# Kernel tuning notes

Measured on AMD Instinct MI355X. Metric: run time of the kernel, lower is better.

## Reference

```python
import jax, jax.numpy as jnp
import numpy as np

MU = 5
ITERATIONS = 3


def _sobel(x):
    # torch kernel: stack([K, K.T]) with K = vertical-gradient Sobel; conv2d is cross-correlation
    k = jnp.array([[-1., -2., -1.], [0., 0., 0.], [1., 2., 1.]], dtype=x.dtype)
    kern = jnp.stack([k, k.T])[:, None]  # [2,1,3,3] -> channels (Gy, Gx)
    return jax.lax.conv_general_dilated(
        x, kern, window_strides=(1, 1), padding=[(1, 1), (1, 1)],
        dimension_numbers=("NCHW", "OIHW", "NCHW"))


def _normalize(v):
    # norm over channel dim, zeros replaced by 1 (matches tang_mag[tang_mag==0]=1)
    mag = jnp.linalg.norm(v, axis=1, keepdims=True)
    mag = jnp.where(mag == 0, jnp.ones_like(mag), mag)
    return v / mag


def etf_forward(inputs, mu=MU, iterations=ITERATIONS):
    B, _, H, W = inputs.shape
    sobel = _sobel(inputs)                                   # [B,2,H,W]
    sobel_mag = jnp.linalg.norm(sobel, axis=1, keepdims=True)
    sobel_mag = sobel_mag / jnp.max(sobel_mag)               # [B,1,H,W]
    pad = lambda t: jnp.pad(t, ((0, 0), (0, 0), (mu, mu), (mu, mu)))
    sobel_mag_padded = pad(sobel_mag)
    sobel_X = sobel_mag
    # tang = sobel.flip(channels) * [-1, 1] => [-Gx, Gy], then normalized
    tang = jnp.stack([-sobel[:, 1], sobel[:, 0]], axis=1)
    tang = _normalize(tang)
    for _ in range(iterations):
        for ori in ("Vertical", "Horizontal"):
            tang_padded = pad(tang)
            tang_X = tang
            acc = jnp.zeros_like(tang)
            for i in range(2 * mu + 1):
                if ori == "Vertical":
                    tang_Y = tang_padded[:, :, i:i + H, mu:mu + W]
                    sobel_Y = sobel_mag_padded[:, :, i:i + H, mu:mu + W]
                else:
                    tang_Y = tang_padded[:, :, mu:mu + H, i:i + W]
                    sobel_Y = sobel_mag_padded[:, :, mu:mu + H, i:i + W]
                w = (jnp.tanh(sobel_Y - sobel_X) + 1.0) * jnp.sum(tang_X * tang_Y, axis=1, keepdims=True) * 0.5
                acc = acc + tang_Y * w
            tang = _normalize(acc)
    return tang


def setup_inputs() -> dict:
    key = jax.random.key(0)
    inputs = jax.random.uniform(key, (2, 1, 1024, 1024), dtype=jnp.float32)
    return {"inputs": inputs}


def reference(inputs) -> jnp.ndarray:
    return etf_forward(inputs)
```

## Files before the change

### kernel.cpp

```cpp
#include <hip/hip_runtime.h>

#define BB 2
#define HH 1024
#define WW 1024
#define MU 5

#define TH 32
#define TW 64
#define SH (TH + 2 * MU)
#define SCW 80
#define SMS 83
#define SVS 81

__device__ __forceinline__ float fast_rcp(float x) { return __builtin_amdgcn_rcpf(x); }
__device__ __forceinline__ float fast_rsq(float x) { return __builtin_amdgcn_rsqf(x); }

#define SR 8
__global__ __launch_bounds__(256) void sobel_init(
    const float* __restrict__ x,
    float* __restrict__ tf,
    float* __restrict__ mag,
    float* __restrict__ block_max)
{
    __shared__ float xs[SR + 2][264];
    const int t = threadIdx.x;
    const int w0 = blockIdx.x * 256;
    const int h0 = blockIdx.y * SR;
    const int b = blockIdx.z;
    const size_t plane = (size_t)HH * WW;
    const float* xb = x + (size_t)b * plane;

    for (int i = t; i < (SR + 2) * 66; i += 256) {
        int r = i / 66, c4 = i % 66;
        int g = h0 - 1 + r;
        int gw = w0 - 4 + 4 * c4;
        float4 v = make_float4(0.f, 0.f, 0.f, 0.f);
        if (g >= 0 && g < HH && gw >= 0 && gw < WW)
            v = *(const float4*)(xb + (size_t)g * WW + gw);
        *(float4*)&xs[r][4 * c4] = v;
    }
    __syncthreads();

    float lmax = 0.f;
    const int c = 4 + t;
    #pragma unroll
    for (int k = 0; k < SR; ++k) {
        const float* rT = xs[k], * rM = xs[k + 1], * rB = xs[k + 2];
        float tl = rT[c - 1], tc = rT[c], tr = rT[c + 1];
        float ml = rM[c - 1],             mr = rM[c + 1];
        float bl = rB[c - 1], bc = rB[c], br = rB[c + 1];
        float s0 = (bl - tl) + 2.f * (bc - tc) + (br - tr);
        float s1 = (tr - tl) + 2.f * (mr - ml) + (br - bl);
        float m = sqrtf(fmaf(s0, s0, s1 * s1));
        float inv = (m == 0.f) ? 1.f : fast_rcp(m);
        size_t gi = (size_t)(h0 + k) * WW + (w0 + t);
        mag[(size_t)b * plane + gi] = m;
        ((float2*)tf)[(size_t)b * plane + gi] = make_float2(-s1 * inv, s0 * inv);
        lmax = fmaxf(lmax, m);
    }

    #pragma unroll
    for (int off = 32; off; off >>= 1) lmax = fmaxf(lmax, __shfl_down(lmax, off, 64));
    __shared__ float smax[4];
    if ((t & 63) == 0) smax[t >> 6] = lmax;
    __syncthreads();
    if (t == 0)
        block_max[(blockIdx.z * 128 + blockIdx.y) * 4 + blockIdx.x] =
            fmaxf(fmaxf(smax[0], smax[1]), fmaxf(smax[2], smax[3]));
}

template <int PLANAR_OUT>
__global__ __launch_bounds__(256, 4) void etf_vh(
    const float* __restrict__ tin,
    float* __restrict__ tout,
    const float* __restrict__ mag,
    const float* __restrict__ block_max)
{
    __shared__ float lds[SH * SCW * 2 + SH * SMS];
    __shared__ float smax[4];
    float* st  = lds;
    float* sm  = lds + SH * SCW * 2;
    float* sv0 = lds;
    float* sv1 = lds + TH * SVS;

    const int t = threadIdx.x;

    int lin = blockIdx.x + 16 * blockIdx.y + 512 * blockIdx.z;
    lin = (lin & 7) * ((16 * 32 * BB) >> 3) + (lin >> 3);
    const int w0 = (lin & 15) * TW;
    const int h0 = ((lin >> 4) & 31) * TH;
    const int b  = lin >> 9;

    const size_t plane = (size_t)HH * WW;
    const float* tb = tin + 2 * (size_t)b * plane;
    const float* mb = mag + (size_t)b * plane;

    {
        float m = fmaxf(fmaxf(block_max[t], block_max[t + 256]),
                        fmaxf(block_max[t + 512], block_max[t + 768]));
        #pragma unroll
        for (int off = 32; off; off >>= 1) m = fmaxf(m, __shfl_down(m, off, 64));
        if ((t & 63) == 0) smax[t >> 6] = m;
    }
    __syncthreads();
    const float gm = fmaxf(fmaxf(smax[0], smax[1]), fmaxf(smax[2], smax[3]));
    const float s2 = 2.f * fast_rcp(gm);

    for (int i = t; i < SH * 40 + SH * 20; i += 256) {
        if (i < SH * 40) {
            int r = i / 40, c4 = i % 40;
            int g = h0 - MU + r;
            int gw = w0 - 8 + 2 * c4;
            float4 v = make_float4(0.f, 0.f, 0.f, 0.f);
            if (g >= 0 && g < HH && gw >= 0 && gw < WW)
                v = *(const float4*)(tb + 2 * ((size_t)g * WW + gw));
            *(float4*)&st[r * (SCW * 2) + 4 * c4] = v;
        } else {
            int j = i - SH * 40;
            int r = j / 20, c4 = j % 20;
            int g = h0 - MU + r;
            int gw = w0 - 8 + 4 * c4;
            float4 v = make_float4(0.f, 0.f, 0.f, 0.f);
            if (g >= 0 && g < HH && gw >= 0 && gw < WW)
                v = *(const float4*)(mb + (size_t)g * WW + gw);
            float* dst = &sm[r * SMS + 4 * c4];
            dst[0] = __expf(-s2 * v.x);
            dst[1] = __expf(-s2 * v.y);
            dst[2] = __expf(-s2 * v.z);
            dst[3] = __expf(-s2 * v.w);
        }
    }
    __syncthreads();

    float r0a[21], r1a[21], rea[21];

    const int c = t % 80;
    const int strip = t / 80;
    const int vr0row = strip * 11;
    const int Rv = (strip == 2) ? 10 : 11;
    if (t < 240) {
        #pragma unroll
        for (int j = 0; j < 21; ++j) {
            if (j < Rv + 10) {
                float2 v = *(const float2*)&st[((vr0row + j) * SCW + c) * 2];
                r0a[j] = v.x; r1a[j] = v.y;
                rea[j] = sm[(vr0row + j) * SMS + c];
            }
        }
    }
    __syncthreads();

    __builtin_amdgcn_s_setprio(1);
    if (t < 240) {
        #pragma unroll
        for (int i = 0; i < 11; ++i) {
            if (i < Rv) {
                float tx0 = r0a[i + 5], tx1 = r1a[i + 5];
                float remx = fast_rcp(rea[i + 5]);
                float a0 = 0.f, a1 = 0.f;
                #pragma unroll
                for (int d = 0; d <= 2 * MU; ++d) {
                    float y0 = r0a[i + d], y1 = r1a[i + d], ey = rea[i + d];
                    float s = fast_rcp(fmaf(ey, remx, 1.f));
                    float w = s * fmaf(tx0, y0, tx1 * y1);
                    a0 = fmaf(y0, w, a0);
                    a1 = fmaf(y1, w, a1);
                }
                float n2 = fmaf(a0, a0, a1 * a1);
                float inv = (n2 == 0.f) ? 1.f : fast_rsq(n2);
                sv0[(vr0row + i) * SVS + c] = a0 * inv;
                sv1[(vr0row + i) * SVS + c] = a1 * inv;
            }
        }
    }
    __builtin_amdgcn_s_setprio(0);
    __syncthreads();

    const int r = t & 31;
    const int cg = t >> 5;
    const int cbase = 8 + cg * 8;
    #pragma unroll
    for (int j = 0; j < 18; ++j) {
        int sc = cbase - 5 + j;
        r0a[j] = sv0[r * SVS + sc];
        r1a[j] = sv1[r * SVS + sc];
        rea[j] = sm[(r + MU) * SMS + sc];
    }
    __syncthreads();

    __builtin_amdgcn_s_setprio(1);
    #pragma unroll
    for (int k = 0; k < 8; ++k) {
        float tx0 = r0a[k + 5], tx1 = r1a[k + 5];
        float remx = fast_rcp(rea[k + 5]);
        float a0 = 0.f, a1 = 0.f;
        #pragma unroll
        for (int d = 0; d <= 2 * MU; ++d) {
            float y0 = r0a[k + d], y1 = r1a[k + d], ey = rea[k + d];
            float s = fast_rcp(fmaf(ey, remx, 1.f));
            float w = s * fmaf(tx0, y0, tx1 * y1);
            a0 = fmaf(y0, w, a0);
            a1 = fmaf(y1, w, a1);
        }
        float n2 = fmaf(a0, a0, a1 * a1);
        float inv = (n2 == 0.f) ? 1.f : fast_rsq(n2);
        sv0[r * SVS + cbase + k] = a0 * inv;
        sv1[r * SVS + cbase + k] = a1 * inv;
    }
    __builtin_amdgcn_s_setprio(0);
    __syncthreads();

    #pragma unroll
    for (int m = 0; m < 8; ++m) {
        int px = t + 256 * m;
        int rr = px >> 6, cc = px & 63;
        float v0 = sv0[rr * SVS + 8 + cc];
        float v1 = sv1[rr * SVS + 8 + cc];
        size_t gi = (size_t)(h0 + rr) * WW + (w0 + cc);
        if (PLANAR_OUT) {
            tout[(size_t)(2 * b)     * plane + gi] = v0;
            tout[(size_t)(2 * b + 1) * plane + gi] = v1;
        } else {
            *(float2*)&tout[2 * ((size_t)b * plane + gi)] = make_float2(v0, v1);
        }
    }
}

extern "C" void kernel_launch(void* const* d_in, const int* in_sizes, int n_in,
                              void* d_out, int out_size, void* d_ws, size_t ws_size,
                              hipStream_t stream)
{
    const float* x = (const float*)d_in[0];
    char* ws = (char*)d_ws;
    const size_t plane = (size_t)HH * WW;

    float* tfA  = (float*)ws;
    float* tfB  = (float*)(ws + sizeof(float) * BB * 2 * plane);
    float* mag  = (float*)(ws + sizeof(float) * BB * 4 * plane);
    float* block_max = (float*)(ws + sizeof(float) * BB * 5 * plane);

    sobel_init<<<dim3(4, 128, BB), 256, 0, stream>>>(x, tfA, mag, block_max);

    dim3 g(WW / TW, HH / TH, BB);
    etf_vh<0><<<g, 256, 0, stream>>>(tfA, tfB, mag, block_max);
    etf_vh<0><<<g, 256, 0, stream>>>(tfB, tfA, mag, block_max);
    etf_vh<1><<<g, 256, 0, stream>>>(tfA, (float*)d_out, mag, block_max);
}
```

Baseline: 131.7 us.

## Fuse Sobel init and three ETF passes into one persistent kernel with grid barriers

Replaces the four kernel launches with a single persistent kernel of 1024 blocks. Each block runs its own Sobel tile and the three ETF passes, with atomic-counter grid barriers between stages. This removes launch gaps and inter-kernel drain/refill overhead. It also trims the tangent halo from 8 to 6 columns to shrink LDS and load volume. It relies on all 1024 blocks being co-resident (4 per CU on 256 CUs) and adds a memset plus a spin-wait with a timeout break, which risks deadlock or incorrect results if occupancy falls short.

```diff
diff --git a/kernel.cpp b/kernel.cpp
--- a/kernel.cpp
+++ b/kernel.cpp
@@ -8,115 +8,54 @@
 #define TH 32
 #define TW 64
 #define SH (TH + 2 * MU)
-#define SCW 80
-#define SMS 83
-#define SVS 81
+#define TCW 78
+#define TST (TCW * 2)
+#define SMS 81
+#define SVS 79
+#define LDSF (SH * TST + SH * SMS)
 
 __device__ __forceinline__ float fast_rcp(float x) { return __builtin_amdgcn_rcpf(x); }
 __device__ __forceinline__ float fast_rsq(float x) { return __builtin_amdgcn_rsqf(x); }
 
-#define SR 8
-__global__ __launch_bounds__(256) void sobel_init(
-    const float* __restrict__ x,
-    float* __restrict__ tf,
-    float* __restrict__ mag,
-    float* __restrict__ block_max)
-{
-    __shared__ float xs[SR + 2][264];
-    const int t = threadIdx.x;
-    const int w0 = blockIdx.x * 256;
-    const int h0 = blockIdx.y * SR;
-    const int b = blockIdx.z;
-    const size_t plane = (size_t)HH * WW;
-    const float* xb = x + (size_t)b * plane;
-
-    for (int i = t; i < (SR + 2) * 66; i += 256) {
-        int r = i / 66, c4 = i % 66;
-        int g = h0 - 1 + r;
-        int gw = w0 - 4 + 4 * c4;
-        float4 v = make_float4(0.f, 0.f, 0.f, 0.f);
-        if (g >= 0 && g < HH && gw >= 0 && gw < WW)
-            v = *(const float4*)(xb + (size_t)g * WW + gw);
-        *(float4*)&xs[r][4 * c4] = v;
-    }
-    __syncthreads();
-
-    float lmax = 0.f;
-    const int c = 4 + t;
-    #pragma unroll
-    for (int k = 0; k < SR; ++k) {
-        const float* rT = xs[k], * rM = xs[k + 1], * rB = xs[k + 2];
-        float tl = rT[c - 1], tc = rT[c], tr = rT[c + 1];
-        float ml = rM[c - 1],             mr = rM[c + 1];
-        float bl = rB[c - 1], bc = rB[c], br = rB[c + 1];
-        float s0 = (bl - tl) + 2.f * (bc - tc) + (br - tr);
-        float s1 = (tr - tl) + 2.f * (mr - ml) + (br - bl);
-        float m = sqrtf(fmaf(s0, s0, s1 * s1));
-        float inv = (m == 0.f) ? 1.f : fast_rcp(m);
-        size_t gi = (size_t)(h0 + k) * WW + (w0 + t);
-        mag[(size_t)b * plane + gi] = m;
-        ((float2*)tf)[(size_t)b * plane + gi] = make_float2(-s1 * inv, s0 * inv);
-        lmax = fmaxf(lmax, m);
-    }
-
-    #pragma unroll
-    for (int off = 32; off; off >>= 1) lmax = fmaxf(lmax, __shfl_down(lmax, off, 64));
-    __shared__ float smax[4];
-    if ((t & 63) == 0) smax[t >> 6] = lmax;
-    __syncthreads();
-    if (t == 0)
-        block_max[(blockIdx.z * 128 + blockIdx.y) * 4 + blockIdx.x] =
-            fmaxf(fmaxf(smax[0], smax[1]), fmaxf(smax[2], smax[3]));
-}
-
-template <int PLANAR_OUT>
-__global__ __launch_bounds__(256, 4) void etf_vh(
-    const float* __restrict__ tin,
-    float* __restrict__ tout,
-    const float* __restrict__ mag,
-    const float* __restrict__ block_max)
-{
-    __shared__ float lds[SH * SCW * 2 + SH * SMS];
-    __shared__ float smax[4];
+__device__ __forceinline__ void gridbar(unsigned* cnt, unsigned target, int t)
+{
+    __syncthreads();
+    if (t == 0) {
+        __hip_atomic_fetch_add(cnt, 1u, __ATOMIC_ACQ_REL, __HIP_MEMORY_SCOPE_AGENT);
+        int spins = 0;
+        while (__hip_atomic_load(cnt, __ATOMIC_ACQUIRE, __HIP_MEMORY_SCOPE_AGENT) < target) {
+            __builtin_amdgcn_s_sleep(2);
+            if (++spins > (1 << 22)) break;
+        }
+    }
+    __syncthreads();
+}
+
+template <int PLANAR>
+__device__ __forceinline__ void etf_pass(
+    float* __restrict__ lds,
+    const float* __restrict__ tb,
+    const float* __restrict__ mb,
+    float* __restrict__ o0,
+    float* __restrict__ o1,
+    float s2, int t, int w0, int h0)
+{
     float* st  = lds;
-    float* sm  = lds + SH * SCW * 2;
+    float* sm  = lds + SH * TST;
     float* sv0 = lds;
     float* sv1 = lds + TH * SVS;
 
-    const int t = threadIdx.x;
-
-    int lin = blockIdx.x + 16 * blockIdx.y + 512 * blockIdx.z;
-    lin = (lin & 7) * ((16 * 32 * BB) >> 3) + (lin >> 3);
-    const int w0 = (lin & 15) * TW;
-    const int h0 = ((lin >> 4) & 31) * TH;
-    const int b  = lin >> 9;
-
-    const size_t plane = (size_t)HH * WW;
-    const float* tb = tin + 2 * (size_t)b * plane;
-    const float* mb = mag + (size_t)b * plane;
-
-    {
-        float m = fmaxf(fmaxf(block_max[t], block_max[t + 256]),
-                        fmaxf(block_max[t + 512], block_max[t + 768]));
-        #pragma unroll
-        for (int off = 32; off; off >>= 1) m = fmaxf(m, __shfl_down(m, off, 64));
-        if ((t & 63) == 0) smax[t >> 6] = m;
-    }
-    __syncthreads();
-    const float gm = fmaxf(fmaxf(smax[0], smax[1]), fmaxf(smax[2], smax[3]));
-    const float s2 = 2.f * fast_rcp(gm);
-
-    for (int i = t; i < SH * 40 + SH * 20; i += 256) {
-        if (i < SH * 40) {
-            int r = i / 40, c4 = i % 40;
+    for (int i = t; i < SH * 39 + SH * 20; i += 256) {
+        if (i < SH * 39) {
+            int r = i / 39, c4 = i % 39;
             int g = h0 - MU + r;
-            int gw = w0 - 8 + 2 * c4;
+            int gw = w0 - 6 + 2 * c4;
             float4 v = make_float4(0.f, 0.f, 0.f, 0.f);
             if (g >= 0 && g < HH && gw >= 0 && gw < WW)
                 v = *(const float4*)(tb + 2 * ((size_t)g * WW + gw));
-            *(float4*)&st[r * (SCW * 2) + 4 * c4] = v;
+            *(float4*)&st[r * TST + 4 * c4] = v;
         } else {
-            int j = i - SH * 40;
+            int j = i - SH * 39;
             int r = j / 20, c4 = j % 20;
             int g = h0 - MU + r;
             int gw = w0 - 8 + 4 * c4;
@@ -134,24 +73,24 @@
 
     float r0a[21], r1a[21], rea[21];
 
-    const int c = t % 80;
-    const int strip = t / 80;
+    const int c = t % TCW;
+    const int strip = t / TCW;
     const int vr0row = strip * 11;
     const int Rv = (strip == 2) ? 10 : 11;
-    if (t < 240) {
+    if (t < 3 * TCW) {
         #pragma unroll
         for (int j = 0; j < 21; ++j) {
             if (j < Rv + 10) {
-                float2 v = *(const float2*)&st[((vr0row + j) * SCW + c) * 2];
+                float2 v = *(const float2*)&st[(vr0row + j) * TST + 2 * c];
                 r0a[j] = v.x; r1a[j] = v.y;
-                rea[j] = sm[(vr0row + j) * SMS + c];
+                rea[j] = sm[(vr0row + j) * SMS + c + 2];
             }
         }
     }
     __syncthreads();
 
     __builtin_amdgcn_s_setprio(1);
-    if (t < 240) {
+    if (t < 3 * TCW) {
         #pragma unroll
         for (int i = 0; i < 11; ++i) {
             if (i < Rv) {
@@ -177,14 +116,14 @@
     __syncthreads();
 
     const int r = t & 31;
-    const int cg = t >> 5;
-    const int cbase = 8 + cg * 8;
+    const int cg_ = t >> 5;
+    const int cbase = 6 + cg_ * 8;
     #pragma unroll
     for (int j = 0; j < 18; ++j) {
         int sc = cbase - 5 + j;
         r0a[j] = sv0[r * SVS + sc];
         r1a[j] = sv1[r * SVS + sc];
-        rea[j] = sm[(r + MU) * SMS + sc];
+        rea[j] = sm[(r + MU) * SMS + sc + 2];
     }
     __syncthreads();
 
@@ -214,16 +153,110 @@
     for (int m = 0; m < 8; ++m) {
         int px = t + 256 * m;
         int rr = px >> 6, cc = px & 63;
-        float v0 = sv0[rr * SVS + 8 + cc];
-        float v1 = sv1[rr * SVS + 8 + cc];
+        float v0 = sv0[rr * SVS + 6 + cc];
+        float v1 = sv1[rr * SVS + 6 + cc];
         size_t gi = (size_t)(h0 + rr) * WW + (w0 + cc);
-        if (PLANAR_OUT) {
-            tout[(size_t)(2 * b)     * plane + gi] = v0;
-            tout[(size_t)(2 * b + 1) * plane + gi] = v1;
+        if (PLANAR) {
+            o0[gi] = v0;
+            o1[gi] = v1;
         } else {
-            *(float2*)&tout[2 * ((size_t)b * plane + gi)] = make_float2(v0, v1);
-        }
-    }
+            *(float2*)&o0[2 * gi] = make_float2(v0, v1);
+        }
+    }
+}
+
+__global__ __launch_bounds__(256, 4) void etf_all(
+    const float* __restrict__ x,
+    float* __restrict__ tfA,
+    float* __restrict__ tfB,
+    float* __restrict__ mag,
+    float* __restrict__ block_max,
+    unsigned* __restrict__ bar,
+    float* __restrict__ out)
+{
+    __shared__ float lds[LDSF];
+    __shared__ float smax[4];
+
+    const int t = threadIdx.x;
+    const int lin0 = blockIdx.x;
+    const int lin = (lin0 & 7) * 128 + (lin0 >> 3);
+    const int w0 = (lin & 15) * TW;
+    const int h0 = ((lin >> 4) & 31) * TH;
+    const int b  = lin >> 9;
+    const size_t plane = (size_t)HH * WW;
+
+    {
+        float* xs = lds;
+        const float* xb = x + (size_t)b * plane;
+        for (int i = t; i < 34 * 18; i += 256) {
+            int r = i / 18, c4 = i % 18;
+            int g = h0 - 1 + r;
+            int gw = w0 - 4 + 4 * c4;
+            float4 v = make_float4(0.f, 0.f, 0.f, 0.f);
+            if (g >= 0 && g < HH && gw >= 0 && gw < WW)
+                v = *(const float4*)(xb + (size_t)g * WW + gw);
+            *(float4*)&xs[r * 76 + 4 * c4] = v;
+        }
+        __syncthreads();
+
+        float lmax = 0.f;
+        const int cc = t & 63;
+        const int rr = t >> 6;
+        const int c = cc + 4;
+        float* mb_w = mag + (size_t)b * plane;
+        float2* tA2 = (float2*)(tfA + 2 * (size_t)b * plane);
+        #pragma unroll
+        for (int k = 0; k < 8; ++k) {
+            int row = rr * 8 + k;
+            const float* rT = &xs[row * 76];
+            const float* rM = rT + 76;
+            const float* rB = rM + 76;
+            float tl = rT[c - 1], tc = rT[c], tr = rT[c + 1];
+            float ml = rM[c - 1],             mr = rM[c + 1];
+            float bl = rB[c - 1], bc = rB[c], br = rB[c + 1];
+            float s0 = (bl - tl) + 2.f * (bc - tc) + (br - tr);
+            float s1 = (tr - tl) + 2.f * (mr - ml) + (br - bl);
+            float m = sqrtf(fmaf(s0, s0, s1 * s1));
+            float inv = (m == 0.f) ? 1.f : fast_rcp(m);
+            size_t gi = (size_t)(h0 + row) * WW + (w0 + cc);
+            mb_w[gi] = m;
+            tA2[gi] = make_float2(-s1 * inv, s0 * inv);
+            lmax = fmaxf(lmax, m);
+        }
+        #pragma unroll
+        for (int off = 32; off; off >>= 1) lmax = fmaxf(lmax, __shfl_down(lmax, off, 64));
+        if ((t & 63) == 0) smax[t >> 6] = lmax;
+        __syncthreads();
+        if (t == 0)
+            block_max[lin0] = fmaxf(fmaxf(smax[0], smax[1]), fmaxf(smax[2], smax[3]));
+    }
+    gridbar(bar, 1024, t);
+
+    float s2;
+    {
+        float m = fmaxf(fmaxf(block_max[t], block_max[t + 256]),
+                        fmaxf(block_max[t + 512], block_max[t + 768]));
+        #pragma unroll
+        for (int off = 32; off; off >>= 1) m = fmaxf(m, __shfl_down(m, off, 64));
+        if ((t & 63) == 0) smax[t >> 6] = m;
+        __syncthreads();
+        const float gm = fmaxf(fmaxf(smax[0], smax[1]), fmaxf(smax[2], smax[3]));
+        s2 = 2.f * fast_rcp(gm);
+    }
+    __syncthreads();
+
+    const float* mb = mag + (size_t)b * plane;
+    float* tA = tfA + 2 * (size_t)b * plane;
+    float* tB = tfB + 2 * (size_t)b * plane;
+
+    etf_pass<0>(lds, tA, mb, tB, nullptr, s2, t, w0, h0);
+    gridbar(bar, 2048, t);
+    etf_pass<0>(lds, tB, mb, tA, nullptr, s2, t, w0, h0);
+    gridbar(bar, 3072, t);
+    etf_pass<1>(lds, tA, mb,
+                out + (size_t)(2 * b) * plane,
+                out + (size_t)(2 * b + 1) * plane,
+                s2, t, w0, h0);
 }
 
 extern "C" void kernel_launch(void* const* d_in, const int* in_sizes, int n_in,
@@ -234,15 +267,14 @@
     char* ws = (char*)d_ws;
     const size_t plane = (size_t)HH * WW;
 
-    float* tfA  = (float*)ws;
-    float* tfB  = (float*)(ws + sizeof(float) * BB * 2 * plane);
-    float* mag  = (float*)(ws + sizeof(float) * BB * 4 * plane);
-    float* block_max = (float*)(ws + sizeof(float) * BB * 5 * plane);
-
-    sobel_init<<<dim3(4, 128, BB), 256, 0, stream>>>(x, tfA, mag, block_max);
-
-    dim3 g(WW / TW, HH / TH, BB);
-    etf_vh<0><<<g, 256, 0, stream>>>(tfA, tfB, mag, block_max);
-    etf_vh<0><<<g, 256, 0, stream>>>(tfB, tfA, mag, block_max);
-    etf_vh<1><<<g, 256, 0, stream>>>(tfA, (float*)d_out, mag, block_max);
-}
+    float* tfA     = (float*)ws;
+    float* tfB     = (float*)(ws + sizeof(float) * BB * 2 * plane);
+    float* mg      = (float*)(ws + sizeof(float) * BB * 4 * plane);
+    float* bmax    = (float*)(ws + sizeof(float) * BB * 5 * plane);
+    unsigned* bar  = (unsigned*)(ws + sizeof(float) * (BB * 5 * plane + 1024));
+
+    hipMemsetAsync(bar, 0, 64, stream);
+
+    etf_all<<<dim3(1024), dim3(256), 0, stream>>>(x, tfA, tfB, mg, bmax, bar,
+                                                  (float*)d_out);
+}
```

Measured after the change: 497.4 us. 278% more time.

## Drop LDS magnitude tile, read magnitudes directly from global with recomputed exp

Applied to the files above, without the earlier changes.

Removes the shared-memory staging of the exponentiated sobel magnitude and instead has each thread load the magnitude from global (cache) and compute the exp in registers for both the vertical and horizontal passes. The tangent halo tile is narrowed from 80 to 78 columns (exact 5-pixel halo) and LDS shrinks, allowing the occupancy hint to rise from 4 to 5 blocks per CU. This trades LDS capacity and a sync-phase fill for redundant exp evaluations and scalar uncoalesced-ish global loads in the horizontal pass.

```diff
diff --git a/kernel.cpp b/kernel.cpp
--- a/kernel.cpp
+++ b/kernel.cpp
@@ -8,12 +8,19 @@
 #define TH 32
 #define TW 64
 #define SH (TH + 2 * MU)
-#define SCW 80
-#define SMS 83
-#define SVS 81
+#define TCW 78
+#define TST (TCW * 2)
+#define SVS 79
+#define LDSF (SH * TST)
 
 __device__ __forceinline__ float fast_rcp(float x) { return __builtin_amdgcn_rcpf(x); }
 __device__ __forceinline__ float fast_rsq(float x) { return __builtin_amdgcn_rsqf(x); }
+
+__device__ __forceinline__ float magat(const float* __restrict__ mb, int g, int gw)
+{
+    return (g >= 0 && g < HH && gw >= 0 && gw < WW)
+         ? mb[(size_t)g * WW + gw] : 0.f;
+}
 
 #define SR 8
 __global__ __launch_bounds__(256) void sobel_init(
@@ -70,16 +77,15 @@
 }
 
 template <int PLANAR_OUT>
-__global__ __launch_bounds__(256, 4) void etf_vh(
+__global__ __launch_bounds__(256, 5) void etf_vh(
     const float* __restrict__ tin,
     float* __restrict__ tout,
     const float* __restrict__ mag,
     const float* __restrict__ block_max)
 {
-    __shared__ float lds[SH * SCW * 2 + SH * SMS];
+    __shared__ float lds[LDSF];
     __shared__ float smax[4];
     float* st  = lds;
-    float* sm  = lds + SH * SCW * 2;
     float* sv0 = lds;
     float* sv1 = lds + TH * SVS;
 
@@ -106,52 +112,37 @@
     const float gm = fmaxf(fmaxf(smax[0], smax[1]), fmaxf(smax[2], smax[3]));
     const float s2 = 2.f * fast_rcp(gm);
 
-    for (int i = t; i < SH * 40 + SH * 20; i += 256) {
-        if (i < SH * 40) {
-            int r = i / 40, c4 = i % 40;
-            int g = h0 - MU + r;
-            int gw = w0 - 8 + 2 * c4;
-            float4 v = make_float4(0.f, 0.f, 0.f, 0.f);
-            if (g >= 0 && g < HH && gw >= 0 && gw < WW)
-                v = *(const float4*)(tb + 2 * ((size_t)g * WW + gw));
-            *(float4*)&st[r * (SCW * 2) + 4 * c4] = v;
-        } else {
-            int j = i - SH * 40;
-            int r = j / 20, c4 = j % 20;
-            int g = h0 - MU + r;
-            int gw = w0 - 8 + 4 * c4;
-            float4 v = make_float4(0.f, 0.f, 0.f, 0.f);
-            if (g >= 0 && g < HH && gw >= 0 && gw < WW)
-                v = *(const float4*)(mb + (size_t)g * WW + gw);
-            float* dst = &sm[r * SMS + 4 * c4];
-            dst[0] = __expf(-s2 * v.x);
-            dst[1] = __expf(-s2 * v.y);
-            dst[2] = __expf(-s2 * v.z);
-            dst[3] = __expf(-s2 * v.w);
-        }
+    for (int i = t; i < SH * 39; i += 256) {
+        int r = i / 39, c4 = i % 39;
+        int g = h0 - MU + r;
+        int gw = w0 - 6 + 2 * c4;
+        float4 v = make_float4(0.f, 0.f, 0.f, 0.f);
+        if (g >= 0 && g < HH && gw >= 0 && gw < WW)
+            v = *(const float4*)(tb + 2 * ((size_t)g * WW + gw));
+        *(float4*)&st[r * TST + 4 * c4] = v;
     }
     __syncthreads();
 
     float r0a[21], r1a[21], rea[21];
 
-    const int c = t % 80;
-    const int strip = t / 80;
+    const int c = t % TCW;
+    const int strip = t / TCW;
     const int vr0row = strip * 11;
     const int Rv = (strip == 2) ? 10 : 11;
-    if (t < 240) {
+    if (t < 3 * TCW) {
         #pragma unroll
         for (int j = 0; j < 21; ++j) {
             if (j < Rv + 10) {
-                float2 v = *(const float2*)&st[((vr0row + j) * SCW + c) * 2];
+                float2 v = *(const float2*)&st[(vr0row + j) * TST + 2 * c];
                 r0a[j] = v.x; r1a[j] = v.y;
-                rea[j] = sm[(vr0row + j) * SMS + c];
+                rea[j] = __expf(-s2 * magat(mb, h0 - MU + vr0row + j, w0 - 6 + c));
             }
         }
     }
     __syncthreads();
 
     __builtin_amdgcn_s_setprio(1);
-    if (t < 240) {
+    if (t < 3 * TCW) {
         #pragma unroll
         for (int i = 0; i < 11; ++i) {
             if (i < Rv) {
@@ -177,14 +168,14 @@
     __syncthreads();
 
     const int r = t & 31;
-    const int cg = t >> 5;
-    const int cbase = 8 + cg * 8;
+    const int cg_ = t >> 5;
+    const int cbase = 6 + cg_ * 8;
     #pragma unroll
     for (int j = 0; j < 18; ++j) {
         int sc = cbase - 5 + j;
         r0a[j] = sv0[r * SVS + sc];
         r1a[j] = sv1[r * SVS + sc];
-        rea[j] = sm[(r + MU) * SMS + sc];
+        rea[j] = __expf(-s2 * magat(mb, h0 + r, w0 + cg_ * 8 - 5 + j));
     }
     __syncthreads();
 
@@ -214,8 +205,8 @@
     for (int m = 0; m < 8; ++m) {
         int px = t + 256 * m;
         int rr = px >> 6, cc = px & 63;
-        float v0 = sv0[rr * SVS + 8 + cc];
-        float v1 = sv1[rr * SVS + 8 + cc];
+        float v0 = sv0[rr * SVS + 6 + cc];
+        float v1 = sv1[rr * SVS + 6 + cc];
         size_t gi = (size_t)(h0 + rr) * WW + (w0 + cc);
         if (PLANAR_OUT) {
             tout[(size_t)(2 * b)     * plane + gi] = v0;
```

After: 139.6 us. 1.06x slower.
